# Kernel optimization log

Measured on AMD Instinct MI355X. Metric: run time of the kernel, lower is better.

The kernel has to match this reference:

```python
import jax, jax.numpy as jnp
import numpy as np


def setup_inputs() -> dict:
    key = jax.random.key(0)
    x = jax.random.normal(key, (64, 1024, 1024), dtype=jnp.float32)
    return {"x": x}


def reference(x):
    # m[b] = x[b] @ x[b]^T  -> [B, d, d]
    m = jnp.einsum('bik,bjk->bij', x, x)
    batch_size = x.shape[0]
    # off-diagonal sum = total sum - trace sum (vectorized diagonal reduction)
    diag_sum = jnp.trace(m, axis1=1, axis2=2).sum()
    return (m.sum() - diag_sum) / batch_size
```

## Files before the change

kernel.cpp:

```cpp
#include <hip/hip_runtime.h>


constexpr int BATCH = 64;
constexpr int DIM   = 1024;
constexpr int ICH   = 8;
constexpr int ROWS  = DIM / ICH;

__device__ __forceinline__ double block_reduce_sum(double v, double* smem) {
    #pragma unroll
    for (int off = 32; off > 0; off >>= 1) v += __shfl_down(v, off, 64);
    const int lane = threadIdx.x & 63;
    const int w    = threadIdx.x >> 6;
    if (lane == 0) smem[w] = v;
    __syncthreads();
    if (threadIdx.x == 0) v = smem[0] + smem[1] + smem[2] + smem[3];
    return v;
}

__global__ __launch_bounds__(256) void ortho_pass1(const float* __restrict__ x,
                                                   float* __restrict__ pcs,
                                                   double* __restrict__ pssq) {
    const int b  = blockIdx.x;
    const int ic = blockIdx.y;
    const int k4 = threadIdx.x * 4;

    const float* xp = x + (size_t)b * DIM * DIM + (size_t)ic * ROWS * DIM + k4;

    float csx = 0.f, csy = 0.f, csz = 0.f, csw = 0.f;
    float ssq = 0.f;
    #pragma unroll 4
    for (int i = 0; i < ROWS; ++i) {
        const float4 v = *reinterpret_cast<const float4*>(xp + (size_t)i * DIM);
        csx += v.x; csy += v.y; csz += v.z; csw += v.w;
        ssq += v.x * v.x + v.y * v.y + v.z * v.z + v.w * v.w;
    }

    float4 cs = make_float4(csx, csy, csz, csw);
    *reinterpret_cast<float4*>(pcs + ((size_t)b * ICH + ic) * DIM + k4) = cs;

    __shared__ double smem[4];
    const double tot = block_reduce_sum((double)ssq, smem);
    if (threadIdx.x == 0) pssq[b * ICH + ic] = tot;
}

__global__ __launch_bounds__(256) void ortho_pass2(const float* __restrict__ pcs,
                                                   double* __restrict__ pbatch) {
    const int b  = blockIdx.x;
    const int k4 = threadIdx.x * 4;

    float tx = 0.f, ty = 0.f, tz = 0.f, tw = 0.f;
    #pragma unroll
    for (int ic = 0; ic < ICH; ++ic) {
        const float4 v = *reinterpret_cast<const float4*>(
            pcs + ((size_t)b * ICH + ic) * DIM + k4);
        tx += v.x; ty += v.y; tz += v.z; tw += v.w;
    }
    const double s = (double)tx * tx + (double)ty * ty
                   + (double)tz * tz + (double)tw * tw;

    __shared__ double smem[4];
    const double tot = block_reduce_sum(s, smem);
    if (threadIdx.x == 0) pbatch[b] = tot;
}

__global__ __launch_bounds__(256) void ortho_pass3(const double* __restrict__ pbatch,
                                                   const double* __restrict__ pssq,
                                                   float* __restrict__ out) {
    double v = 0.0;
    for (int i = threadIdx.x; i < BATCH; i += 256) v += pbatch[i];
    double q = 0.0;
    for (int i = threadIdx.x; i < BATCH * ICH; i += 256) q += pssq[i];

    __shared__ double smem[4];
    const double sv = block_reduce_sum(v, smem);
    __syncthreads();
    const double sq = block_reduce_sum(q, smem);
    if (threadIdx.x == 0) out[0] = (float)((sv - sq) / (double)BATCH);
}

extern "C" void kernel_launch(void* const* d_in, const int* in_sizes, int n_in,
                              void* d_out, int out_size, void* d_ws, size_t ws_size,
                              hipStream_t stream) {
    const float* x = (const float*)d_in[0];
    float* out = (float*)d_out;

    float*  pcs    = (float*)d_ws;
    double* pssq   = (double*)((char*)d_ws + sizeof(float) * (size_t)BATCH * ICH * DIM);
    double* pbatch = pssq + BATCH * ICH;

    ortho_pass1<<<dim3(BATCH, ICH), 256, 0, stream>>>(x, pcs, pssq);
    ortho_pass2<<<BATCH, 256, 0, stream>>>(pcs, pbatch);
    ortho_pass3<<<1, 256, 0, stream>>>(pbatch, pssq, out);
}
```

Measured before the change: 50.18 us.

## Fuse column-sum and squaring passes into one kernel with LDS team reduction

Merges the per-chunk column-sum pass and the per-batch squaring pass into a single kernel. Each block covers a quarter of the columns of one batch with eight waves splitting the rows, and combines their partial column sums in shared memory. This removes one kernel launch and the global round-trip of partial column sums, and deepens the load unroll. The trade-off is narrower contiguous row segments per wave and one block per batch-quarter.

```diff
diff --git a/kernel.cpp b/kernel.cpp
--- a/kernel.cpp
+++ b/kernel.cpp
@@ -3,79 +3,70 @@
 
 constexpr int BATCH = 64;
 constexpr int DIM   = 1024;
-constexpr int ICH   = 8;
-constexpr int ROWS  = DIM / ICH;
+constexpr int KR    = 4;
+constexpr int COLS  = DIM / KR;
+constexpr int TEAMS = 8;
+constexpr int TROWS = DIM / TEAMS;
 
-__device__ __forceinline__ double block_reduce_sum(double v, double* smem) {
-    #pragma unroll
-    for (int off = 32; off > 0; off >>= 1) v += __shfl_down(v, off, 64);
+__global__ __launch_bounds__(512) void ortho_main(const float* __restrict__ x,
+                                                  double* __restrict__ part) {
+    const int b    = blockIdx.x / KR;
+    const int kr   = blockIdx.x % KR;
     const int lane = threadIdx.x & 63;
-    const int w    = threadIdx.x >> 6;
-    if (lane == 0) smem[w] = v;
-    __syncthreads();
-    if (threadIdx.x == 0) v = smem[0] + smem[1] + smem[2] + smem[3];
-    return v;
-}
+    const int team = threadIdx.x >> 6;
 
-__global__ __launch_bounds__(256) void ortho_pass1(const float* __restrict__ x,
-                                                   float* __restrict__ pcs,
-                                                   double* __restrict__ pssq) {
-    const int b  = blockIdx.x;
-    const int ic = blockIdx.y;
-    const int k4 = threadIdx.x * 4;
-
-    const float* xp = x + (size_t)b * DIM * DIM + (size_t)ic * ROWS * DIM + k4;
+    const float* xp = x + (size_t)b * DIM * DIM + (size_t)team * TROWS * DIM
+                        + (size_t)kr * COLS + (size_t)lane * 4;
 
     float csx = 0.f, csy = 0.f, csz = 0.f, csw = 0.f;
     float ssq = 0.f;
-    #pragma unroll 4
-    for (int i = 0; i < ROWS; ++i) {
+    #pragma unroll 8
+    for (int i = 0; i < TROWS; ++i) {
         const float4 v = *reinterpret_cast<const float4*>(xp + (size_t)i * DIM);
         csx += v.x; csy += v.y; csz += v.z; csw += v.w;
         ssq += v.x * v.x + v.y * v.y + v.z * v.z + v.w * v.w;
     }
 
-    float4 cs = make_float4(csx, csy, csz, csw);
-    *reinterpret_cast<float4*>(pcs + ((size_t)b * ICH + ic) * DIM + k4) = cs;
+    __shared__ float sc[TEAMS][COLS];
+    sc[team][lane * 4 + 0] = csx;
+    sc[team][lane * 4 + 1] = csy;
+    sc[team][lane * 4 + 2] = csz;
+    sc[team][lane * 4 + 3] = csw;
+    __syncthreads();
 
-    __shared__ double smem[4];
-    const double tot = block_reduce_sum((double)ssq, smem);
-    if (threadIdx.x == 0) pssq[b * ICH + ic] = tot;
+    double val = -(double)ssq;
+    if (threadIdx.x < COLS) {
+        float c = 0.f;
+        #pragma unroll
+        for (int t = 0; t < TEAMS; ++t) c += sc[t][threadIdx.x];
+        val += (double)c * (double)c;
+    }
+
+    #pragma unroll
+    for (int off = 32; off > 0; off >>= 1) val += __shfl_down(val, off, 64);
+    __shared__ double sred[TEAMS];
+    if (lane == 0) sred[team] = val;
+    __syncthreads();
+    if (threadIdx.x == 0) {
+        double t = 0.0;
+        #pragma unroll
+        for (int i = 0; i < TEAMS; ++i) t += sred[i];
+        part[blockIdx.x] = t;
+    }
 }
 
-__global__ __launch_bounds__(256) void ortho_pass2(const float* __restrict__ pcs,
-                                                   double* __restrict__ pbatch) {
-    const int b  = blockIdx.x;
-    const int k4 = threadIdx.x * 4;
-
-    float tx = 0.f, ty = 0.f, tz = 0.f, tw = 0.f;
+__global__ __launch_bounds__(256) void ortho_final(const double* __restrict__ part,
+                                                   float* __restrict__ out) {
+    double v = part[threadIdx.x];
     #pragma unroll
-    for (int ic = 0; ic < ICH; ++ic) {
-        const float4 v = *reinterpret_cast<const float4*>(
-            pcs + ((size_t)b * ICH + ic) * DIM + k4);
-        tx += v.x; ty += v.y; tz += v.z; tw += v.w;
-    }
-    const double s = (double)tx * tx + (double)ty * ty
-                   + (double)tz * tz + (double)tw * tw;
-
-    __shared__ double smem[4];
-    const double tot = block_reduce_sum(s, smem);
-    if (threadIdx.x == 0) pbatch[b] = tot;
-}
-
-__global__ __launch_bounds__(256) void ortho_pass3(const double* __restrict__ pbatch,
-                                                   const double* __restrict__ pssq,
-                                                   float* __restrict__ out) {
-    double v = 0.0;
-    for (int i = threadIdx.x; i < BATCH; i += 256) v += pbatch[i];
-    double q = 0.0;
-    for (int i = threadIdx.x; i < BATCH * ICH; i += 256) q += pssq[i];
-
-    __shared__ double smem[4];
-    const double sv = block_reduce_sum(v, smem);
+    for (int off = 32; off > 0; off >>= 1) v += __shfl_down(v, off, 64);
+    __shared__ double sred[4];
+    const int lane = threadIdx.x & 63;
+    const int w    = threadIdx.x >> 6;
+    if (lane == 0) sred[w] = v;
     __syncthreads();
-    const double sq = block_reduce_sum(q, smem);
-    if (threadIdx.x == 0) out[0] = (float)((sv - sq) / (double)BATCH);
+    if (threadIdx.x == 0)
+        out[0] = (float)((sred[0] + sred[1] + sred[2] + sred[3]) / (double)BATCH);
 }
 
 extern "C" void kernel_launch(void* const* d_in, const int* in_sizes, int n_in,
@@ -83,12 +74,8 @@
                               hipStream_t stream) {
     const float* x = (const float*)d_in[0];
     float* out = (float*)d_out;
+    double* part = (double*)d_ws;
 
-    float*  pcs    = (float*)d_ws;
-    double* pssq   = (double*)((char*)d_ws + sizeof(float) * (size_t)BATCH * ICH * DIM);
-    double* pbatch = pssq + BATCH * ICH;
-
-    ortho_pass1<<<dim3(BATCH, ICH), 256, 0, stream>>>(x, pcs, pssq);
-    ortho_pass2<<<BATCH, 256, 0, stream>>>(pcs, pbatch);
-    ortho_pass3<<<1, 256, 0, stream>>>(pbatch, pssq, out);
+    ortho_main<<<BATCH * KR, 512, 0, stream>>>(x, part);
+    ortho_final<<<1, 256, 0, stream>>>(part, out);
 }
```

Result: faster. 45.74 us (-8.8%).
